# Performance work log

Measured on AMD Instinct MI355X. Metric: run time of the kernel, lower is better.

The kernel has to match this reference:

```python
import jax, jax.numpy as jnp
import numpy as np

OUT_FEATURES = 4096
IN_FEATURES = 4096
NNZ = 1048576
BATCH = 128


def setup_inputs() -> dict:
    key = jax.random.key(0)
    k_x, k_v, k_r, k_c = jax.random.split(key, 4)
    X = jax.random.normal(k_x, (BATCH, IN_FEATURES), dtype=jnp.float32)
    W_vals = jax.random.normal(k_v, (NNZ,), dtype=jnp.float32)
    W_rows = jax.random.randint(k_r, (NNZ,), 0, OUT_FEATURES, dtype=jnp.int32)
    W_cols = jax.random.randint(k_c, (NNZ,), 0, IN_FEATURES, dtype=jnp.int32)
    return {"X": X, "W_vals": W_vals, "W_rows": W_rows, "W_cols": W_cols}


def reference(X, W_vals, W_rows, W_cols):
    # torch.sparse.mm(W, X.T).T with W in COO form.
    # out[b, i] = sum_{k: rows[k]==i} vals[k] * X[b, cols[k]]
    gathered = X.T[W_cols] * W_vals[:, None]            # [nnz, B]
    out_T = jax.ops.segment_sum(gathered, W_rows, num_segments=OUT_FEATURES)  # [OUT, B]
    return out_T.T                                       # [B, OUT]
```

## Files before the change

### kernel.cpp

```cpp
#include <hip/hip_runtime.h>
#include <hip/hip_bf16.h>

#define OUTF 4096
#define INF  4096
#define BATCH 128
#define NBIN 512
#define CAP  48
#define NSLAB 8

typedef _Float16 f16x8 __attribute__((ext_vector_type(8)));
typedef float    f32x4 __attribute__((ext_vector_type(4)));

__global__ __launch_bounds__(256) void k_cvtX(const float* __restrict__ X,
                                              _Float16* __restrict__ Xh) {
  int g = blockIdx.x * 256 + threadIdx.x;
  int n = g >> 9;
  int k0 = (g & 511) * 8;
  float4 f0 = *(const float4*)(X + (size_t)n * INF + k0);
  float4 f1 = *(const float4*)(X + (size_t)n * INF + k0 + 4);
  f16x8 h;
  h[0] = (_Float16)f0.x; h[1] = (_Float16)f0.y;
  h[2] = (_Float16)f0.z; h[3] = (_Float16)f0.w;
  h[4] = (_Float16)f1.x; h[5] = (_Float16)f1.y;
  h[6] = (_Float16)f1.z; h[7] = (_Float16)f1.w;
  size_t idx = ((size_t)(k0 >> 5) * 8 + (n >> 4)) * 512 + (n & 15) * 32 + (k0 & 31);
  *(f16x8*)(Xh + idx) = h;
}

__global__ __launch_bounds__(256) void k_bin(const float* __restrict__ vals,
                                             const int* __restrict__ rows,
                                             const int* __restrict__ cols, int nnz,
                                             int2* __restrict__ bucket,
                                             int* __restrict__ cnts) {
  __shared__ int cnt[NBIN];
  const int t = threadIdx.x;
  const int blk = blockIdx.x;
  for (int b = t; b < NBIN; b += 256) cnt[b] = 0;
  __syncthreads();

  const int G4 = nnz >> 2;
  for (int g = blk * 256 + t; g < G4; g += 256 * 256) {
    int4   r4 = ((const int4*)rows)[g];
    int4   c4 = ((const int4*)cols)[g];
    float4 v4 = ((const float4*)vals)[g];
    int rr[4] = {r4.x, r4.y, r4.z, r4.w};
    int cc[4] = {c4.x, c4.y, c4.z, c4.w};
    float vv[4] = {v4.x, v4.y, v4.z, v4.w};
#pragma unroll
    for (int j = 0; j < 4; ++j) {
      int bin = ((rr[j] >> 4) << 1) | (cc[j] >> 11);
      int slot = atomicAdd(&cnt[bin], 1);
      if (slot < CAP) {
        int2 e;
        e.x = __float_as_int(vv[j]);
        e.y = ((rr[j] & 15) << 11) | (cc[j] & 2047);
        bucket[((size_t)bin * 256 + blk) * CAP + slot] = e;
      }
    }
  }
  if (blk == 0 && t < (nnz & 3)) {
    int i = (G4 << 2) + t;
    int r = rows[i], c = cols[i];
    int bin = ((r >> 4) << 1) | (c >> 11);
    int slot = atomicAdd(&cnt[bin], 1);
    if (slot < CAP) {
      int2 e;
      e.x = __float_as_int(vals[i]);
      e.y = ((r & 15) << 11) | (c & 2047);
      bucket[((size_t)bin * 256 + blk) * CAP + slot] = e;
    }
  }
  __syncthreads();
  for (int b = t; b < NBIN; b += 256)
    cnts[blk * NBIN + b] = min(cnt[b], CAP);
}

#define SSTRIDE 2052
__global__ __launch_bounds__(256, 1) void k_strip(const int2* __restrict__ bucket,
                                                  const int* __restrict__ cnts,
                                                  const _Float16* __restrict__ Xh,
                                                  float* __restrict__ outP) {
  __shared__ float strip[16 * SSTRIDE];
  const int t = threadIdx.x;
  const int bin = blockIdx.x;
  const int mt = bin >> 1, khalf = bin & 1;

  {
    float4 z = {0.f, 0.f, 0.f, 0.f};
    const int nvec = 16 * SSTRIDE / 4;
    for (int j = t; j < nvec; j += 256) ((float4*)strip)[j] = z;
  }
  __syncthreads();

  {
    int cnt = cnts[t * NBIN + bin];
    const int2* cell = bucket + ((size_t)bin * 256 + t) * CAP;
    for (int j = 0; j < cnt; ++j) {
      int2 e = cell[j];
      int lr4 = (e.y >> 11) & 15;
      int kc  = e.y & 2047;
      atomicAdd(&strip[lr4 * SSTRIDE + kc], __int_as_float(e.x));
    }
  }
  __syncthreads();

  const int lane = t & 63, wid = t >> 6;
  const int lr = lane & 15, lg = lane >> 4;
  f32x4 acc[8] = {};
#pragma unroll 2
  for (int ktl = wid; ktl < 64; ktl += 4) {
    const int kt = khalf * 64 + ktl;
    float4 alo = *(const float4*)&strip[lr * SSTRIDE + ktl * 32 + lg * 8];
    float4 ahi = *(const float4*)&strip[lr * SSTRIDE + ktl * 32 + lg * 8 + 4];
    f16x8 a;
    a[0] = (_Float16)alo.x; a[1] = (_Float16)alo.y;
    a[2] = (_Float16)alo.z; a[3] = (_Float16)alo.w;
    a[4] = (_Float16)ahi.x; a[5] = (_Float16)ahi.y;
    a[6] = (_Float16)ahi.z; a[7] = (_Float16)ahi.w;
    const _Float16* bp = Xh + (size_t)kt * 8 * 512 + lr * 32 + lg * 8;
    f16x8 b[8];
#pragma unroll
    for (int nt = 0; nt < 8; ++nt) b[nt] = *(const f16x8*)(bp + nt * 512);
#pragma unroll
    for (int nt = 0; nt < 8; ++nt)
      acc[nt] = __builtin_amdgcn_mfma_f32_16x16x32_f16(a, b[nt], acc[nt], 0, 0, 0);
  }

  float* op = outP + (size_t)(khalf * 4 + wid) * (OUTF * BATCH) + mt * 2048;
#pragma unroll
  for (int nt = 0; nt < 8; ++nt)
#pragma unroll
    for (int i = 0; i < 4; ++i)
      op[(size_t)(lg * 4 + i) * 128 + nt * 16 + lr] = acc[nt][i];
}

__global__ __launch_bounds__(1024) void k_merge(const float* __restrict__ outP,
                                                float* __restrict__ out) {
  __shared__ float t[32][33];
  int bbase = blockIdx.x * 32;
  int rbase = blockIdx.y * 32;
  size_t src = (size_t)(rbase + threadIdx.y) * 128 + bbase + threadIdx.x;
  float s = 0.f;
#pragma unroll
  for (int sl = 0; sl < NSLAB; ++sl)
    s += outP[(size_t)sl * OUTF * BATCH + src];
  t[threadIdx.y][threadIdx.x] = s;
  __syncthreads();
  out[(size_t)(bbase + threadIdx.y) * OUTF + rbase + threadIdx.x] = t[threadIdx.x][threadIdx.y];
}

__global__ __launch_bounds__(256) void k_fallback(const float* __restrict__ X,
                                                  const float* __restrict__ vals,
                                                  const int* __restrict__ rows,
                                                  const int* __restrict__ cols, int n,
                                                  float* __restrict__ out) {
  int k = blockIdx.x * blockDim.x + threadIdx.x;
  if (k >= n) return;
  float v = vals[k];
  int r = rows[k], c = cols[k];
  for (int b = 0; b < BATCH; ++b)
    atomicAdd(&out[(size_t)b * OUTF + r], v * X[(size_t)b * INF + c]);
}

extern "C" void kernel_launch(void* const* d_in, const int* in_sizes, int n_in,
                              void* d_out, int out_size, void* d_ws, size_t ws_size,
                              hipStream_t stream) {
  const float* X  = (const float*)d_in[0];
  const float* Wv = (const float*)d_in[1];
  const int*   Wr = (const int*)d_in[2];
  const int*   Wc = (const int*)d_in[3];
  float* out = (float*)d_out;
  const int nnz = in_sizes[1];

  char* ws = (char*)d_ws;
  const size_t OFF_XH   = 0;
  const size_t OFF_BKT  = OFF_XH  + (size_t)BATCH * INF * 2;
  const size_t OFF_CNT  = OFF_BKT + (size_t)NBIN * 256 * CAP * 8;
  const size_t OFF_OUTP = OFF_CNT + (size_t)256 * NBIN * 4;
  const size_t NEEDED   = OFF_OUTP + (size_t)NSLAB * OUTF * BATCH * 4;

  if (ws_size < NEEDED) {
    hipMemsetAsync(d_out, 0, (size_t)out_size * 4, stream);
    k_fallback<<<dim3((nnz + 255) / 256), dim3(256), 0, stream>>>(X, Wv, Wr, Wc, nnz, out);
    return;
  }

  _Float16* Xh     = (_Float16*)(ws + OFF_XH);
  int2*     bucket = (int2*)(ws + OFF_BKT);
  int*      cnts   = (int*)(ws + OFF_CNT);
  float*    outP   = (float*)(ws + OFF_OUTP);

  k_cvtX<<<dim3(BATCH * INF / (256 * 8)), dim3(256), 0, stream>>>(X, Xh);
  k_bin<<<dim3(256), dim3(256), 0, stream>>>(Wv, Wr, Wc, nnz, bucket, cnts);
  k_strip<<<dim3(NBIN), dim3(256), 0, stream>>>(bucket, cnts, Xh, outP);
  k_merge<<<dim3(BATCH / 32, OUTF / 32), dim3(32, 32), 0, stream>>>(outP, out);
}
```

Baseline: 112.2 us.

## Fuse X conversion into binning and split strips into K-quarters with in-block reduction

```diff
diff --git a/kernel.cpp b/kernel.cpp
--- a/kernel.cpp
+++ b/kernel.cpp
@@ -4,102 +4,103 @@
 #define OUTF 4096
 #define INF  4096
 #define BATCH 128
-#define NBIN 512
-#define CAP  48
-#define NSLAB 8
+#define NBIN 1024
+#define NCELL 1024
+#define CAP  16
+#define SQ   1028
 
 typedef _Float16 f16x8 __attribute__((ext_vector_type(8)));
 typedef float    f32x4 __attribute__((ext_vector_type(4)));
 
-__global__ __launch_bounds__(256) void k_cvtX(const float* __restrict__ X,
-                                              _Float16* __restrict__ Xh) {
-  int g = blockIdx.x * 256 + threadIdx.x;
-  int n = g >> 9;
-  int k0 = (g & 511) * 8;
-  float4 f0 = *(const float4*)(X + (size_t)n * INF + k0);
-  float4 f1 = *(const float4*)(X + (size_t)n * INF + k0 + 4);
-  f16x8 h;
-  h[0] = (_Float16)f0.x; h[1] = (_Float16)f0.y;
-  h[2] = (_Float16)f0.z; h[3] = (_Float16)f0.w;
-  h[4] = (_Float16)f1.x; h[5] = (_Float16)f1.y;
-  h[6] = (_Float16)f1.z; h[7] = (_Float16)f1.w;
-  size_t idx = ((size_t)(k0 >> 5) * 8 + (n >> 4)) * 512 + (n & 15) * 32 + (k0 & 31);
-  *(f16x8*)(Xh + idx) = h;
-}
 
-__global__ __launch_bounds__(256) void k_bin(const float* __restrict__ vals,
-                                             const int* __restrict__ rows,
-                                             const int* __restrict__ cols, int nnz,
-                                             int2* __restrict__ bucket,
-                                             int* __restrict__ cnts) {
+__global__ __launch_bounds__(256) void k_prep(const float* __restrict__ X,
+                                              const float* __restrict__ vals,
+                                              const int* __restrict__ rows,
+                                              const int* __restrict__ cols, int nnz,
+                                              _Float16* __restrict__ Xh,
+                                              int2* __restrict__ bucket,
+                                              int* __restrict__ cnts) {
   __shared__ int cnt[NBIN];
   const int t = threadIdx.x;
   const int blk = blockIdx.x;
-  for (int b = t; b < NBIN; b += 256) cnt[b] = 0;
-  __syncthreads();
-
-  const int G4 = nnz >> 2;
-  for (int g = blk * 256 + t; g < G4; g += 256 * 256) {
-    int4   r4 = ((const int4*)rows)[g];
-    int4   c4 = ((const int4*)cols)[g];
-    float4 v4 = ((const float4*)vals)[g];
-    int rr[4] = {r4.x, r4.y, r4.z, r4.w};
-    int cc[4] = {c4.x, c4.y, c4.z, c4.w};
-    float vv[4] = {v4.x, v4.y, v4.z, v4.w};
+  if (blk < NCELL) {
+    for (int b = t; b < NBIN; b += 256) cnt[b] = 0;
+    __syncthreads();
+    const int G4 = nnz >> 2;
+    const int g = blk * 256 + t;
+    if (g < G4) {
+      int4   r4 = ((const int4*)rows)[g];
+      int4   c4 = ((const int4*)cols)[g];
+      float4 v4 = ((const float4*)vals)[g];
+      int rr[4] = {r4.x, r4.y, r4.z, r4.w};
+      int cc[4] = {c4.x, c4.y, c4.z, c4.w};
+      float vv[4] = {v4.x, v4.y, v4.z, v4.w};
 #pragma unroll
-    for (int j = 0; j < 4; ++j) {
-      int bin = ((rr[j] >> 4) << 1) | (cc[j] >> 11);
-      int slot = atomicAdd(&cnt[bin], 1);
-      if (slot < CAP) {
-        int2 e;
-        e.x = __float_as_int(vv[j]);
-        e.y = ((rr[j] & 15) << 11) | (cc[j] & 2047);
-        bucket[((size_t)bin * 256 + blk) * CAP + slot] = e;
+      for (int j = 0; j < 4; ++j) {
+        int bin = ((rr[j] >> 4) << 2) | (cc[j] >> 10);
+        int slot = atomicAdd(&cnt[bin], 1);
+        if (slot < CAP) {
+          int2 e;
+          e.x = __float_as_int(vv[j]);
+          e.y = ((rr[j] & 15) << 10) | (cc[j] & 1023);
+          bucket[((size_t)blk * NBIN + bin) * CAP + slot] = e;
+        }
       }
     }
+    if (blk == 0) {
+      for (int i = (nnz & ~3) + t; i < nnz; i += 256) {
+        int r = rows[i], c = cols[i];
+        int bin = ((r >> 4) << 2) | (c >> 10);
+        int slot = atomicAdd(&cnt[bin], 1);
+        if (slot < CAP) {
+          int2 e;
+          e.x = __float_as_int(vals[i]);
+          e.y = ((r & 15) << 10) | (c & 1023);
+          bucket[((size_t)blk * NBIN + bin) * CAP + slot] = e;
+        }
+      }
+    }
+    __syncthreads();
+    for (int b = t; b < NBIN; b += 256)
+      cnts[(size_t)blk * NBIN + b] = min(cnt[b], CAP);
+  } else {
+    int g = (blk - NCELL) * 256 + t;
+    int n = g >> 9;
+    int k0 = (g & 511) * 8;
+    float4 f0 = *(const float4*)(X + (size_t)n * INF + k0);
+    float4 f1 = *(const float4*)(X + (size_t)n * INF + k0 + 4);
+    f16x8 h;
+    h[0] = (_Float16)f0.x; h[1] = (_Float16)f0.y;
+    h[2] = (_Float16)f0.z; h[3] = (_Float16)f0.w;
+    h[4] = (_Float16)f1.x; h[5] = (_Float16)f1.y;
+    h[6] = (_Float16)f1.z; h[7] = (_Float16)f1.w;
+    size_t idx = ((size_t)(k0 >> 5) * 8 + (n >> 4)) * 512 + (n & 15) * 32 + (k0 & 31);
+    *(f16x8*)(Xh + idx) = h;
   }
-  if (blk == 0 && t < (nnz & 3)) {
-    int i = (G4 << 2) + t;
-    int r = rows[i], c = cols[i];
-    int bin = ((r >> 4) << 1) | (c >> 11);
-    int slot = atomicAdd(&cnt[bin], 1);
-    if (slot < CAP) {
-      int2 e;
-      e.x = __float_as_int(vals[i]);
-      e.y = ((r & 15) << 11) | (c & 2047);
-      bucket[((size_t)bin * 256 + blk) * CAP + slot] = e;
-    }
-  }
-  __syncthreads();
-  for (int b = t; b < NBIN; b += 256)
-    cnts[blk * NBIN + b] = min(cnt[b], CAP);
 }
 
-#define SSTRIDE 2052
-__global__ __launch_bounds__(256, 1) void k_strip(const int2* __restrict__ bucket,
+__global__ __launch_bounds__(256, 2) void k_strip(const int2* __restrict__ bucket,
                                                   const int* __restrict__ cnts,
                                                   const _Float16* __restrict__ Xh,
                                                   float* __restrict__ outP) {
-  __shared__ float strip[16 * SSTRIDE];
+  __shared__ float strip[16 * SQ];
   const int t = threadIdx.x;
   const int bin = blockIdx.x;
-  const int mt = bin >> 1, khalf = bin & 1;
+  const int mt = bin >> 2, kq = bin & 3;
 
   {
     float4 z = {0.f, 0.f, 0.f, 0.f};
-    const int nvec = 16 * SSTRIDE / 4;
+    const int nvec = 16 * SQ / 4;
     for (int j = t; j < nvec; j += 256) ((float4*)strip)[j] = z;
   }
   __syncthreads();
 
-  {
-    int cnt = cnts[t * NBIN + bin];
-    const int2* cell = bucket + ((size_t)bin * 256 + t) * CAP;
+  for (int cc = t; cc < NCELL; cc += 256) {
+    int cnt = cnts[(size_t)cc * NBIN + bin];
+    const int2* cell = bucket + ((size_t)cc * NBIN + bin) * CAP;
     for (int j = 0; j < cnt; ++j) {
       int2 e = cell[j];
-      int lr4 = (e.y >> 11) & 15;
-      int kc  = e.y & 2047;
-      atomicAdd(&strip[lr4 * SSTRIDE + kc], __int_as_float(e.x));
+      atomicAdd(&strip[((e.y >> 10) & 15) * SQ + (e.y & 1023)], __int_as_float(e.x));
     }
   }
   __syncthreads();
@@ -107,17 +108,16 @@
   const int lane = t & 63, wid = t >> 6;
   const int lr = lane & 15, lg = lane >> 4;
   f32x4 acc[8] = {};
-#pragma unroll 2
-  for (int ktl = wid; ktl < 64; ktl += 4) {
-    const int kt = khalf * 64 + ktl;
-    float4 alo = *(const float4*)&strip[lr * SSTRIDE + ktl * 32 + lg * 8];
-    float4 ahi = *(const float4*)&strip[lr * SSTRIDE + ktl * 32 + lg * 8 + 4];
+  for (int ktl = wid; ktl < 32; ktl += 4) {
+    const int kt = kq * 32 + ktl;
+    float4 alo = *(const float4*)&strip[lr * SQ + ktl * 32 + lg * 8];
+    float4 ahi = *(const float4*)&strip[lr * SQ + ktl * 32 + lg * 8 + 4];
     f16x8 a;
     a[0] = (_Float16)alo.x; a[1] = (_Float16)alo.y;
     a[2] = (_Float16)alo.z; a[3] = (_Float16)alo.w;
     a[4] = (_Float16)ahi.x; a[5] = (_Float16)ahi.y;
     a[6] = (_Float16)ahi.z; a[7] = (_Float16)ahi.w;
-    const _Float16* bp = Xh + (size_t)kt * 8 * 512 + lr * 32 + lg * 8;
+    const _Float16* bp = Xh + (size_t)kt * 4096 + lr * 32 + lg * 8;
     f16x8 b[8];
 #pragma unroll
     for (int nt = 0; nt < 8; ++nt) b[nt] = *(const f16x8*)(bp + nt * 512);
@@ -125,13 +125,18 @@
     for (int nt = 0; nt < 8; ++nt)
       acc[nt] = __builtin_amdgcn_mfma_f32_16x16x32_f16(a, b[nt], acc[nt], 0, 0, 0);
   }
+  __syncthreads();
 
-  float* op = outP + (size_t)(khalf * 4 + wid) * (OUTF * BATCH) + mt * 2048;
+  float* red = strip;
 #pragma unroll
   for (int nt = 0; nt < 8; ++nt)
 #pragma unroll
     for (int i = 0; i < 4; ++i)
-      op[(size_t)(lg * 4 + i) * 128 + nt * 16 + lr] = acc[nt][i];
+      red[wid * 2048 + (lg * 4 + i) * 128 + nt * 16 + lr] = acc[nt][i];
+  __syncthreads();
+  float* op = outP + (size_t)kq * (OUTF * BATCH) + (size_t)mt * 2048;
+  for (int e = t; e < 2048; e += 256)
+    op[e] = red[e] + red[2048 + e] + red[4096 + e] + red[6144 + e];
 }
 
 __global__ __launch_bounds__(1024) void k_merge(const float* __restrict__ outP,
@@ -140,10 +145,8 @@
   int bbase = blockIdx.x * 32;
   int rbase = blockIdx.y * 32;
   size_t src = (size_t)(rbase + threadIdx.y) * 128 + bbase + threadIdx.x;
-  float s = 0.f;
-#pragma unroll
-  for (int sl = 0; sl < NSLAB; ++sl)
-    s += outP[(size_t)sl * OUTF * BATCH + src];
+  float s = outP[src] + outP[(size_t)OUTF * BATCH + src] +
+            outP[(size_t)2 * OUTF * BATCH + src] + outP[(size_t)3 * OUTF * BATCH + src];
   t[threadIdx.y][threadIdx.x] = s;
   __syncthreads();
   out[(size_t)(bbase + threadIdx.y) * OUTF + rbase + threadIdx.x] = t[threadIdx.x][threadIdx.y];
@@ -175,9 +178,9 @@
   char* ws = (char*)d_ws;
   const size_t OFF_XH   = 0;
   const size_t OFF_BKT  = OFF_XH  + (size_t)BATCH * INF * 2;
-  const size_t OFF_CNT  = OFF_BKT + (size_t)NBIN * 256 * CAP * 8;
-  const size_t OFF_OUTP = OFF_CNT + (size_t)256 * NBIN * 4;
-  const size_t NEEDED   = OFF_OUTP + (size_t)NSLAB * OUTF * BATCH * 4;
+  const size_t OFF_CNT  = OFF_BKT + (size_t)NCELL * NBIN * CAP * 8;
+  const size_t OFF_OUTP = OFF_CNT + (size_t)NCELL * NBIN * 4;
+  const size_t NEEDED   = OFF_OUTP + (size_t)4 * OUTF * BATCH * 4;
 
   if (ws_size < NEEDED) {
     hipMemsetAsync(d_out, 0, (size_t)out_size * 4, stream);
@@ -190,8 +193,7 @@
   int*      cnts   = (int*)(ws + OFF_CNT);
   float*    outP   = (float*)(ws + OFF_OUTP);
 
-  k_cvtX<<<dim3(BATCH * INF / (256 * 8)), dim3(256), 0, stream>>>(X, Xh);
-  k_bin<<<dim3(256), dim3(256), 0, stream>>>(Wv, Wr, Wc, nnz, bucket, cnts);
+  k_prep<<<dim3(NCELL + 256), dim3(256), 0, stream>>>(X, Wv, Wr, Wc, nnz, Xh, bucket, cnts);
   k_strip<<<dim3(NBIN), dim3(256), 0, stream>>>(bucket, cnts, Xh, outP);
   k_merge<<<dim3(BATCH / 32, OUTF / 32), dim3(32, 32), 0, stream>>>(outP, out);
 }
```

Result: slower. 122.2 us (+8.9%).
